# Performance work log

Hardware: AMD Instinct MI355X
Metric: run time of the kernel (lower is better)

## Reference

```python
import jax, jax.numpy as jnp
import numpy as np

LAGRANGE_ORDER = 5  # fixed, as in the torch module


def _lagrange_weights(alpha):
    """Vectorised Lagrange weights of length L+1. alpha: [B,N] -> [B,N,L+1]."""
    L = LAGRANGE_ORDER
    j = jnp.arange(L + 1, dtype=alpha.dtype)
    u = alpha[..., None] - j                          # [B,N,L+1]
    denom = j[:, None] - j[None, :]                   # [L+1,L+1]
    mask = ~jnp.eye(L + 1, dtype=bool)
    num = jnp.where(mask, u[..., None, :], jnp.ones_like(u)[..., None, :])
    den = jnp.where(mask, denom, jnp.ones_like(denom))
    return (num / den).prod(axis=-1)                  # [B,N,L+1]


def setup_inputs() -> dict:
    key = jax.random.key(0)
    k1, k2, k3 = jax.random.split(key, 3)
    B, N = 16, 16384
    # fractional period in samples, in [40, 100) -> max floor(f0)=99, K=99+5+3=107<=108
    f0 = 40.0 + 60.0 * jax.random.uniform(k1, (B, N), dtype=jnp.float32)
    x = jax.random.normal(k2, (B, N), dtype=jnp.float32)
    l_b = jax.random.uniform(k3, (B, N, 2), dtype=jnp.float32)  # (g, p) in [0,1]
    return {"f0": f0, "x": x, "l_b": l_b, "K": 108}


def reference(f0, x, l_b, K):
    B, N = x.shape
    L = LAGRANGE_ORDER
    # design_loop: (g, p) -> loop taps [b0, a1]; gain capped <1 for stability
    g = 0.99 * l_b[..., 0]
    p = l_b[..., 1]
    b0 = g * (1.0 - p)                                # [B,N]
    a1 = g * p
    # tune_f0: subtract low-frequency phase delay of (b0 + a1 z^-1)
    f0c = f0 - a1 / (b0 + a1 + 1e-7)
    # Lagrange centre & weights
    z = jnp.floor(f0c).astype(jnp.int32)
    z_center = z - L // 2                             # [B,N]
    alpha = f0c - z_center.astype(f0.dtype)
    w = _lagrange_weights(alpha)                      # [B,N,L+1]
    # compute_resonator_matrix: loop filter convolved with fractional delay -> block [B,N,L+2]
    block = (b0[..., None] * jnp.pad(w, ((0, 0), (0, 0), (0, 1)))
             + a1[..., None] * jnp.pad(w, ((0, 0), (0, 0), (1, 0))))
    # scatter (-block) into A; LPC lag k+1 lives in column k
    cols = z_center[..., None] - 1 + jnp.arange(L + 2)  # [B,N,L+2]
    cols = jnp.clip(cols, 0, K - 1)
    A = jnp.zeros((B, N, K), x.dtype).at[
        jnp.arange(B)[:, None, None], jnp.arange(N)[None, :, None], cols
    ].add(-block)
    # sample_wise_lpc: y[n] = x[n] - sum_k A[n,k] * y[n-1-k], zero init state
    def step(buf, inp):
        a_n, x_n = inp                                 # [B,K], [B]
        y_n = x_n - jnp.sum(a_n * buf, axis=-1)
        buf = jnp.concatenate([y_n[:, None], buf[:, :-1]], axis=1)
        return buf, y_n
    buf0 = jnp.zeros((B, K), x.dtype)
    _, ys = jax.lax.scan(step, buf0, (A.transpose(1, 0, 2), x.T))  # ys: [N,B]
    return ys.T
```

## Files before the change

### kernel.cpp

```cpp
#include <hip/hip_runtime.h>
#include <math.h>


#define B_    16
#define N_    16384
#define S_    16
#define NSEG  1024
#define NITER 28
#define RUNS  104
#define CHUNK 37

#define TG_FLOATS (B_ * S_ * RUNS * RUNS)
#define ST_FLOATS (B_ * S_ * RUNS)

__device__ __forceinline__ void diffks_coeffs(float f0v, float lbg, float lbp,
                                              int n, float4& lo, float4& hi) {
  float g  = 0.99f * lbg;
  float p  = lbp;
  float b0 = g * (1.0f - p);
  float a1 = g * p;
  float f0c = f0v - a1 / (b0 + a1 + 1e-7f);
  int   zc  = (int)floorf(f0c) - 2;
  float alpha = f0c - (float)zc;
  float u0 = alpha;
  float u1 = alpha - 1.0f;
  float u2 = alpha - 2.0f;
  float u3 = alpha - 3.0f;
  float u4 = alpha - 4.0f;
  float u5 = alpha - 5.0f;
  float w0 = u1 * u2 * u3 * u4 * u5 * (-1.0f / 120.0f);
  float w1 = u0 * u2 * u3 * u4 * u5 * ( 1.0f /  24.0f);
  float w2 = u0 * u1 * u3 * u4 * u5 * (-1.0f /  12.0f);
  float w3 = u0 * u1 * u2 * u4 * u5 * ( 1.0f /  12.0f);
  float w4 = u0 * u1 * u2 * u3 * u5 * (-1.0f /  24.0f);
  float w5 = u0 * u1 * u2 * u3 * u4 * ( 1.0f / 120.0f);
  lo.x = b0 * w0;
  lo.y = fmaf(b0, w1, a1 * w0);
  lo.z = fmaf(b0, w2, a1 * w1);
  lo.w = fmaf(b0, w3, a1 * w2);
  hi.x = fmaf(b0, w4, a1 * w3);
  hi.y = fmaf(b0, w5, a1 * w4);
  hi.z = a1 * w5;
  hi.w = __int_as_float((n - 6 - zc) & 255);
}

__global__ __launch_bounds__(1024) void diffks_phase1(
    const float* __restrict__ f0, const float* __restrict__ lb,
    const float* __restrict__ x, float* __restrict__ Tg) {
  const int bs = blockIdx.x;
  const int b  = bs >> 4, s = bs & 15;
  const int n0 = s << 10;
  const int tid = threadIdx.x;

  __shared__ __align__(16) float hist[256 * RUNS];
  __shared__ float4 sLo[NSEG], sHi[NSEG];
  __shared__ float  sX[NSEG];

  {
    const size_t gi = (size_t)b * N_ + n0 + tid;
    float4 lo, hi;
    diffks_coeffs(f0[gi], lb[2 * gi], lb[2 * gi + 1], tid, lo, hi);
    sLo[tid] = lo; sHi[tid] = hi; sX[tid] = x[gi];
  }
  for (int i = tid; i < 64 * RUNS; i += 1024)
    ((float4*)hist)[i] = float4{0.0f, 0.0f, 0.0f, 0.0f};
  __syncthreads();
  if (tid < 103) hist[(255 - tid) * RUNS + tid] = 1.0f;
  __syncthreads();

  const int w    = tid >> 6;
  const int lane = tid & 63;
  const int cl   = 2 * lane;
  const bool act = (lane < 52);
  const bool px  = (lane == 51);

  for (int t = 0; t < 32; ++t) {
#pragma unroll
    for (int u = 0; u < 2; ++u) {
      const int p = 32 * t + 2 * w + u;
      const float4 lo = sLo[p];
      const float4 hi = sHi[p];
      const float  xv = sX[p];
      if (act) {
        const int base = __float_as_int(hi.w);
        float2 acc;
        acc.x = 0.0f;
        acc.y = px ? xv : 0.0f;
        const float c[7] = {hi.z, hi.y, hi.x, lo.w, lo.z, lo.y, lo.x};
#pragma unroll
        for (int m = 0; m < 7; ++m) {
          const int row = (base + m) & 255;
          const float2 v = *(const float2*)&hist[row * RUNS + cl];
          acc.x = fmaf(c[m], v.x, acc.x);
          acc.y = fmaf(c[m], v.y, acc.y);
        }
        *(float2*)&hist[(p & 255) * RUNS + cl] = acc;
      }
    }
    __syncthreads();
  }

  float* __restrict__ T = Tg + (size_t)bs * RUNS * RUNS;
  for (int idx = tid; idx < RUNS * RUNS; idx += 1024) {
    const int r = idx / RUNS;
    const int j = idx - r * RUNS;
    T[idx] = (j < 103) ? hist[((255 - j) & 255) * RUNS + r] : 0.0f;
  }
}

#define P2_STEP(s_, tv_)                                                      \
  {                                                                           \
    if (q == 0) states[((size_t)b * S_ + (s_)) * RUNS + j] = cur[j];          \
    float acc = 0.0f;                                                         \
    _Pragma("unroll")                                                         \
    for (int k = 0; k < 13; ++k) acc = fmaf(tv_[k], cur[r0 + k], acc);        \
    if ((s_) + 2 < S_) {                                                      \
      const float* __restrict__ Tn = Tb + (size_t)((s_) + 2) * RUNS * RUNS;   \
      _Pragma("unroll")                                                       \
      for (int k = 0; k < 13; ++k) tv_[k] = Tn[(size_t)(r0 + k) * RUNS + j];  \
    }                                                                         \
    part[q][j] = acc;                                                         \
    __syncthreads();                                                          \
    if (q == 0) {                                                             \
      float v = 0.0f;                                                         \
      _Pragma("unroll")                                                       \
      for (int qq = 0; qq < 8; ++qq) v += part[qq][j];                        \
      cur[j] = (j < 103) ? v : 1.0f;                                          \
    }                                                                         \
    __syncthreads();                                                          \
  }

__global__ __launch_bounds__(832) void diffks_phase2(
    const float* __restrict__ Tg, float* __restrict__ states) {
  const int b   = blockIdx.x;
  const int tid = threadIdx.x;
  const int j   = tid % RUNS;
  const int q   = tid / RUNS;
  const int r0  = 13 * q;
  __shared__ float cur[RUNS];
  __shared__ float part[8][105];
  if (tid < 103) cur[tid] = 0.0f;
  if (tid == 103) cur[103] = 1.0f;
  __syncthreads();

  const float* __restrict__ Tb = Tg + (size_t)b * S_ * RUNS * RUNS;
  float tvA[13], tvB[13];
#pragma unroll
  for (int k = 0; k < 13; ++k)
    tvA[k] = Tb[(size_t)(r0 + k) * RUNS + j];
#pragma unroll
  for (int k = 0; k < 13; ++k)
    tvB[k] = Tb[(size_t)RUNS * RUNS + (size_t)(r0 + k) * RUNS + j];

#pragma unroll
  for (int sp = 0; sp < 8; ++sp) {
    P2_STEP(2 * sp,     tvA)
    P2_STEP(2 * sp + 1, tvB)
  }
}

__global__ __launch_bounds__(256) void diffks_phase3(
    const float* __restrict__ f0, const float* __restrict__ lb,
    const float* __restrict__ x, const float* __restrict__ states,
    float* __restrict__ y) {
  const int bs = blockIdx.x;
  const int b  = bs >> 4, s = bs & 15;
  const int n0 = s << 10;
  const int tid = threadIdx.x;

  __shared__ __align__(16) float ring[512];
  __shared__ float4 sC[2 * NSEG];
  __shared__ float  sX[NSEG];
  __shared__ float  sY[NSEG];

#pragma unroll
  for (int k = 0; k < 2; ++k) ring[tid + 256 * k] = 0.0f;
  {
    const size_t gb = (size_t)b * N_ + n0;
    const float*  __restrict__ f0b = f0 + gb;
    const float2* __restrict__ lbb = (const float2*)(lb + 2 * gb);
    const float*  __restrict__ xb  = x + gb;
    float  vf[4]; float2 vl[4]; float vx[4];
#pragma unroll
    for (int k = 0; k < 4; ++k) {
      const int i = tid + 256 * k;
      vf[k] = f0b[i]; vl[k] = lbb[i]; vx[k] = xb[i];
    }
#pragma unroll
    for (int k = 0; k < 4; ++k) {
      const int i = tid + 256 * k;
      float4 lo, hi;
      diffks_coeffs(vf[k], vl[k].x, vl[k].y, n0 + i, lo, hi);
      sC[2 * i] = lo; sC[2 * i + 1] = hi; sX[i] = vx[k];
    }
  }
  __syncthreads();
  const float* __restrict__ st = states + (size_t)bs * RUNS;
  if (tid < 103) {
    const float v = st[tid];
    ring[255 - tid] = v;
    ring[511 - tid] = v;
  }
  __syncthreads();

  if (tid < 64) {
    const int lane = tid;
    const bool act = (lane < CHUNK);
    for (int t = 0; t < NITER; ++t) {
      const int p = t * CHUNK + lane;
      if (act && p < NSEG) {
        const float4 lo = sC[2 * p];
        const float4 hi = sC[2 * p + 1];
        const float  xv = sX[p];
        const int base = __float_as_int(hi.w);
        const float r0 = ring[base + 0];
        const float r1 = ring[base + 1];
        const float r2 = ring[base + 2];
        const float r3 = ring[base + 3];
        const float r4 = ring[base + 4];
        const float r5 = ring[base + 5];
        const float r6 = ring[base + 6];
        const float s0 = fmaf(lo.x, r6, xv);
        const float s1 = fmaf(lo.y, r5, lo.z * r4);
        const float s2 = fmaf(lo.w, r3, hi.x * r2);
        const float s3 = fmaf(hi.y, r1, hi.z * r0);
        const float yv = (s0 + s1) + (s2 + s3);
        const int wsl = p & 255;
        ring[wsl]       = yv;
        ring[wsl + 256] = yv;
        sY[p] = yv;
      }
      __builtin_amdgcn_wave_barrier();
      asm volatile("" ::: "memory");
    }
  }
  __syncthreads();

  float4* __restrict__ yb = (float4*)(y + (size_t)b * N_ + n0);
  yb[tid] = ((const float4*)sY)[tid];
}

__global__ __launch_bounds__(256) void diffks_coeff_fb(
    const float* __restrict__ f0, const float* __restrict__ lb,
    float* __restrict__ cw, int total, int Nmask) {
  int idx = blockIdx.x * blockDim.x + threadIdx.x;
  if (idx >= total) return;
  float4 lo, hi;
  diffks_coeffs(f0[idx], lb[2 * idx], lb[2 * idx + 1], idx & Nmask, lo, hi);
  float4* out4 = (float4*)cw;
  out4[2 * idx]     = lo;
  out4[2 * idx + 1] = hi;
}

__global__ __launch_bounds__(64) void diffks_scan_fb(
    const float* __restrict__ x, const float* __restrict__ cw,
    float* __restrict__ y, int N) {
  const int b    = blockIdx.x;
  const int lane = threadIdx.x;
  __shared__ float ring[512];
#pragma unroll
  for (int i = 0; i < 8; ++i) ring[lane + 64 * i] = 0.0f;
  __builtin_amdgcn_wave_barrier();
  asm volatile("" ::: "memory");
  const float4* __restrict__ c4 = (const float4*)(cw + (size_t)b * N * 8);
  const float*  __restrict__ xb = x + (size_t)b * N;
  float*        __restrict__ yb = y + (size_t)b * N;
  const bool act = (lane < CHUNK);
  const int nIter = (N + CHUNK - 1) / CHUNK;
  for (int t = 0; t < nIter; ++t) {
    const int n = t * CHUNK + lane;
    if (act && n < N) {
      const float4 lo = c4[2 * n];
      const float4 hi = c4[2 * n + 1];
      const float  xv = xb[n];
      const int base = __float_as_int(hi.w);
      const float r0 = ring[base + 0];
      const float r1 = ring[base + 1];
      const float r2 = ring[base + 2];
      const float r3 = ring[base + 3];
      const float r4 = ring[base + 4];
      const float r5 = ring[base + 5];
      const float r6 = ring[base + 6];
      const float s0 = fmaf(lo.x, r6, xv);
      const float s1 = fmaf(lo.y, r5, lo.z * r4);
      const float s2 = fmaf(lo.w, r3, hi.x * r2);
      const float s3 = fmaf(hi.y, r1, hi.z * r0);
      const float yv = (s0 + s1) + (s2 + s3);
      ring[n & 255]         = yv;
      ring[(n & 255) + 256] = yv;
      yb[n] = yv;
    }
    __builtin_amdgcn_wave_barrier();
    asm volatile("" ::: "memory");
  }
}

extern "C" void kernel_launch(void* const* d_in, const int* in_sizes, int n_in,
                              void* d_out, int out_size, void* d_ws, size_t ws_size,
                              hipStream_t stream) {
  const float* f0 = (const float*)d_in[0];
  const float* x  = (const float*)d_in[1];
  const float* lb = (const float*)d_in[2];
  float* out = (float*)d_out;

  const int total = in_sizes[0];
  const size_t need = (size_t)(TG_FLOATS + ST_FLOATS) * 4;

  if (total == B_ * N_ && ws_size >= need) {
    float* Tg = (float*)d_ws;
    float* st = Tg + TG_FLOATS;
    diffks_phase1<<<B_ * S_, 1024, 0, stream>>>(f0, lb, x, Tg);
    diffks_phase2<<<B_, 832, 0, stream>>>(Tg, st);
    diffks_phase3<<<B_ * S_, 256, 0, stream>>>(f0, lb, x, st, out);
  } else {
    const int N = total / B_;
    float* cw = (float*)d_ws;
    diffks_coeff_fb<<<(total + 255) / 256, 256, 0, stream>>>(f0, lb, cw, total, N - 1);
    diffks_scan_fb<<<B_, 64, 0, stream>>>(x, cw, out, N);
  }
}
```

Measured before the change: 104.7 us.

## Fuse three-phase scan into one kernel with global atomic flag handoff

Merges the three kernels (segment transfer matrices, cross-segment state propagation, per-segment final scan) into a single launch of 256 blocks. Blocks signal completion through monotonically increasing global counters compared against snapshots taken at kernel start. The last segment block of each batch runs the state propagation and the other blocks spin-wait for their incoming state. The aim is to remove two kernel launch gaps and reuse the coefficients already held in shared memory. In exchange it relies on all 256 blocks being co-resident to avoid deadlock, and it serializes the phase-2 work onto one block per batch.

Result: slower. 176.1 us (+68.2%).

```diff
diff --git a/kernel.cpp b/kernel.cpp
--- a/kernel.cpp
+++ b/kernel.cpp
@@ -12,6 +12,7 @@
 
 #define TG_FLOATS (B_ * S_ * RUNS * RUNS)
 #define ST_FLOATS (B_ * S_ * RUNS)
+#define NFLAGS    512
 
 __device__ __forceinline__ void diffks_coeffs(float f0v, float lbg, float lbp,
                                               int n, float4& lo, float4& hi) {
@@ -44,84 +45,26 @@
   hi.w = __int_as_float((n - 6 - zc) & 255);
 }
 
-__global__ __launch_bounds__(1024) void diffks_phase1(
-    const float* __restrict__ f0, const float* __restrict__ lb,
-    const float* __restrict__ x, float* __restrict__ Tg) {
-  const int bs = blockIdx.x;
-  const int b  = bs >> 4, s = bs & 15;
-  const int n0 = s << 10;
-  const int tid = threadIdx.x;
-
-  __shared__ __align__(16) float hist[256 * RUNS];
-  __shared__ float4 sLo[NSEG], sHi[NSEG];
-  __shared__ float  sX[NSEG];
-
-  {
-    const size_t gi = (size_t)b * N_ + n0 + tid;
-    float4 lo, hi;
-    diffks_coeffs(f0[gi], lb[2 * gi], lb[2 * gi + 1], tid, lo, hi);
-    sLo[tid] = lo; sHi[tid] = hi; sX[tid] = x[gi];
-  }
-  for (int i = tid; i < 64 * RUNS; i += 1024)
-    ((float4*)hist)[i] = float4{0.0f, 0.0f, 0.0f, 0.0f};
-  __syncthreads();
-  if (tid < 103) hist[(255 - tid) * RUNS + tid] = 1.0f;
-  __syncthreads();
-
-  const int w    = tid >> 6;
-  const int lane = tid & 63;
-  const int cl   = 2 * lane;
-  const bool act = (lane < 52);
-  const bool px  = (lane == 51);
-
-  for (int t = 0; t < 32; ++t) {
-#pragma unroll
-    for (int u = 0; u < 2; ++u) {
-      const int p = 32 * t + 2 * w + u;
-      const float4 lo = sLo[p];
-      const float4 hi = sHi[p];
-      const float  xv = sX[p];
-      if (act) {
-        const int base = __float_as_int(hi.w);
-        float2 acc;
-        acc.x = 0.0f;
-        acc.y = px ? xv : 0.0f;
-        const float c[7] = {hi.z, hi.y, hi.x, lo.w, lo.z, lo.y, lo.x};
-#pragma unroll
-        for (int m = 0; m < 7; ++m) {
-          const int row = (base + m) & 255;
-          const float2 v = *(const float2*)&hist[row * RUNS + cl];
-          acc.x = fmaf(c[m], v.x, acc.x);
-          acc.y = fmaf(c[m], v.y, acc.y);
-        }
-        *(float2*)&hist[(p & 255) * RUNS + cl] = acc;
-      }
-    }
-    __syncthreads();
-  }
-
-  float* __restrict__ T = Tg + (size_t)bs * RUNS * RUNS;
-  for (int idx = tid; idx < RUNS * RUNS; idx += 1024) {
-    const int r = idx / RUNS;
-    const int j = idx - r * RUNS;
-    T[idx] = (j < 103) ? hist[((255 - j) & 255) * RUNS + r] : 0.0f;
-  }
-}
-
-#define P2_STEP(s_, tv_)                                                      \
+#define P2F_STEP(s_, tv_)                                                     \
   {                                                                           \
-    if (q == 0) states[((size_t)b * S_ + (s_)) * RUNS + j] = cur[j];          \
-    float acc = 0.0f;                                                         \
-    _Pragma("unroll")                                                         \
-    for (int k = 0; k < 13; ++k) acc = fmaf(tv_[k], cur[r0 + k], acc);        \
-    if ((s_) + 2 < S_) {                                                      \
-      const float* __restrict__ Tn = Tb + (size_t)((s_) + 2) * RUNS * RUNS;   \
+    if (p2a) {                                                                \
+      if (q == 0) states[((size_t)b * S_ + (s_)) * RUNS + j] = cur[j];        \
+      float acc = 0.0f;                                                       \
       _Pragma("unroll")                                                       \
-      for (int k = 0; k < 13; ++k) tv_[k] = Tn[(size_t)(r0 + k) * RUNS + j];  \
+      for (int k = 0; k < 13; ++k) acc = fmaf(tv_[k], cur[r0 + k], acc);      \
+      if ((s_) + 2 < S_) {                                                    \
+        const float* __restrict__ Tn = Tb + (size_t)((s_) + 2) * RUNS * RUNS; \
+        _Pragma("unroll")                                                     \
+        for (int k = 0; k < 13; ++k) tv_[k] = Tn[(size_t)(r0 + k) * RUNS + j];\
+      }                                                                       \
+      part[q][j] = acc;                                                       \
     }                                                                         \
-    part[q][j] = acc;                                                         \
     __syncthreads();                                                          \
-    if (q == 0) {                                                             \
+    if (tid == 0) {                                                           \
+      __threadfence();                                                        \
+      atomicAdd(&flagS[(b << 4) + (s_)], 1u);                                 \
+    }                                                                         \
+    if (p2a && q == 0) {                                                      \
       float v = 0.0f;                                                         \
       _Pragma("unroll")                                                       \
       for (int qq = 0; qq < 8; ++qq) v += part[qq][j];                        \
@@ -130,87 +73,161 @@
     __syncthreads();                                                          \
   }
 
-__global__ __launch_bounds__(832) void diffks_phase2(
-    const float* __restrict__ Tg, float* __restrict__ states) {
-  const int b   = blockIdx.x;
-  const int tid = threadIdx.x;
-  const int j   = tid % RUNS;
-  const int q   = tid / RUNS;
-  const int r0  = 13 * q;
-  __shared__ float cur[RUNS];
-  __shared__ float part[8][105];
-  if (tid < 103) cur[tid] = 0.0f;
-  if (tid == 103) cur[103] = 1.0f;
-  __syncthreads();
-
-  const float* __restrict__ Tb = Tg + (size_t)b * S_ * RUNS * RUNS;
-  float tvA[13], tvB[13];
-#pragma unroll
-  for (int k = 0; k < 13; ++k)
-    tvA[k] = Tb[(size_t)(r0 + k) * RUNS + j];
-#pragma unroll
-  for (int k = 0; k < 13; ++k)
-    tvB[k] = Tb[(size_t)RUNS * RUNS + (size_t)(r0 + k) * RUNS + j];
-
-#pragma unroll
-  for (int sp = 0; sp < 8; ++sp) {
-    P2_STEP(2 * sp,     tvA)
-    P2_STEP(2 * sp + 1, tvB)
-  }
-}
-
-__global__ __launch_bounds__(256) void diffks_phase3(
+__global__ __launch_bounds__(1024) void diffks_fused(
     const float* __restrict__ f0, const float* __restrict__ lb,
-    const float* __restrict__ x, const float* __restrict__ states,
-    float* __restrict__ y) {
+    const float* __restrict__ x, float* __restrict__ Tg,
+    float* __restrict__ states, unsigned* __restrict__ flagT,
+    unsigned* __restrict__ flagS, float* __restrict__ y) {
   const int bs = blockIdx.x;
   const int b  = bs >> 4, s = bs & 15;
   const int n0 = s << 10;
   const int tid = threadIdx.x;
 
-  __shared__ __align__(16) float ring[512];
-  __shared__ float4 sC[2 * NSEG];
+  __shared__ __align__(16) float hist[256 * RUNS];
+  __shared__ __align__(16) float4 sLo[NSEG], sHi[NSEG];
   __shared__ float  sX[NSEG];
-  __shared__ float  sY[NSEG];
-
-#pragma unroll
-  for (int k = 0; k < 2; ++k) ring[tid + 256 * k] = 0.0f;
+  __shared__ unsigned snapT[16];
+
+  unsigned snapS = 0u;
+  if (tid == 0)
+    snapS = __hip_atomic_load(&flagS[bs], __ATOMIC_RELAXED,
+                              __HIP_MEMORY_SCOPE_AGENT);
+  if (tid < 16)
+    snapT[tid] = __hip_atomic_load(&flagT[(b << 4) + tid], __ATOMIC_RELAXED,
+                                   __HIP_MEMORY_SCOPE_AGENT);
+
   {
-    const size_t gb = (size_t)b * N_ + n0;
-    const float*  __restrict__ f0b = f0 + gb;
-    const float2* __restrict__ lbb = (const float2*)(lb + 2 * gb);
-    const float*  __restrict__ xb  = x + gb;
-    float  vf[4]; float2 vl[4]; float vx[4];
-#pragma unroll
-    for (int k = 0; k < 4; ++k) {
-      const int i = tid + 256 * k;
-      vf[k] = f0b[i]; vl[k] = lbb[i]; vx[k] = xb[i];
-    }
-#pragma unroll
-    for (int k = 0; k < 4; ++k) {
-      const int i = tid + 256 * k;
-      float4 lo, hi;
-      diffks_coeffs(vf[k], vl[k].x, vl[k].y, n0 + i, lo, hi);
-      sC[2 * i] = lo; sC[2 * i + 1] = hi; sX[i] = vx[k];
-    }
-  }
-  __syncthreads();
-  const float* __restrict__ st = states + (size_t)bs * RUNS;
-  if (tid < 103) {
-    const float v = st[tid];
-    ring[255 - tid] = v;
-    ring[511 - tid] = v;
+    const size_t gi = (size_t)b * N_ + n0 + tid;
+    float4 lo, hi;
+    diffks_coeffs(f0[gi], lb[2 * gi], lb[2 * gi + 1], tid, lo, hi);
+    sLo[tid] = lo; sHi[tid] = hi; sX[tid] = x[gi];
+  }
+  for (int i = tid; i < 64 * RUNS; i += 1024)
+    ((float4*)hist)[i] = float4{0.0f, 0.0f, 0.0f, 0.0f};
+  __syncthreads();
+  if (tid < 103) hist[(255 - tid) * RUNS + tid] = 1.0f;
+  __syncthreads();
+
+  {
+    const int w    = tid >> 6;
+    const int lane = tid & 63;
+    const int cl   = 2 * lane;
+    const bool act = (lane < 52);
+    const bool px  = (lane == 51);
+
+    for (int t = 0; t < 32; ++t) {
+#pragma unroll
+      for (int u = 0; u < 2; ++u) {
+        const int p = 32 * t + 2 * w + u;
+        const float4 lo = sLo[p];
+        const float4 hi = sHi[p];
+        const float  xv = sX[p];
+        if (act) {
+          const int base = __float_as_int(hi.w);
+          float2 acc;
+          acc.x = 0.0f;
+          acc.y = px ? xv : 0.0f;
+          const float c[7] = {hi.z, hi.y, hi.x, lo.w, lo.z, lo.y, lo.x};
+#pragma unroll
+          for (int m = 0; m < 7; ++m) {
+            const int row = (base + m) & 255;
+            const float2 v = *(const float2*)&hist[row * RUNS + cl];
+            acc.x = fmaf(c[m], v.x, acc.x);
+            acc.y = fmaf(c[m], v.y, acc.y);
+          }
+          *(float2*)&hist[(p & 255) * RUNS + cl] = acc;
+        }
+      }
+      __syncthreads();
+    }
+  }
+
+  {
+    float* __restrict__ T = Tg + (size_t)bs * RUNS * RUNS;
+    for (int idx = tid; idx < RUNS * RUNS; idx += 1024) {
+      const int r = idx / RUNS;
+      const int j = idx - r * RUNS;
+      T[idx] = (j < 103) ? hist[((255 - j) & 255) * RUNS + r] : 0.0f;
+    }
+  }
+  __syncthreads();
+  if (tid == 0) {
+    __threadfence();
+    atomicAdd(&flagT[bs], 1u);
+  }
+
+  if (tid < 512) hist[tid] = 0.0f;
+
+  if (s == 15) {
+    if (tid == 0) {
+      for (int i = 0; i < 16; ++i) {
+        while (__hip_atomic_load(&flagT[(b << 4) + i], __ATOMIC_RELAXED,
+                                 __HIP_MEMORY_SCOPE_AGENT) == snapT[i])
+          __builtin_amdgcn_s_sleep(1);
+      }
+      __threadfence();
+    }
+    __syncthreads();
+
+    const int j   = tid % RUNS;
+    const int q   = tid / RUNS;
+    const int r0  = 13 * q;
+    const bool p2a = (tid < 832);
+    float* __restrict__ cur = hist + 1536;
+    float (*__restrict__ part)[105] = (float (*)[105])(hist + 1664);
+
+    if (tid < 103) cur[tid] = 0.0f;
+    if (tid == 103) cur[103] = 1.0f;
+    __syncthreads();
+
+    const float* __restrict__ Tb = Tg + (size_t)b * S_ * RUNS * RUNS;
+    float tvA[13], tvB[13];
+    if (p2a) {
+#pragma unroll
+      for (int k = 0; k < 13; ++k)
+        tvA[k] = Tb[(size_t)(r0 + k) * RUNS + j];
+#pragma unroll
+      for (int k = 0; k < 13; ++k)
+        tvB[k] = Tb[(size_t)RUNS * RUNS + (size_t)(r0 + k) * RUNS + j];
+    }
+
+#pragma unroll
+    for (int sp = 0; sp < 8; ++sp) {
+      P2F_STEP(2 * sp,     tvA)
+      P2F_STEP(2 * sp + 1, tvB)
+    }
+  }
+
+  if (s != 15 && s != 0) {
+    if (tid == 0) {
+      while (__hip_atomic_load(&flagS[bs], __ATOMIC_RELAXED,
+                               __HIP_MEMORY_SCOPE_AGENT) == snapS)
+        __builtin_amdgcn_s_sleep(1);
+      __threadfence();
+    }
+  }
+  __syncthreads();
+
+  if (s != 0) {
+    const float* __restrict__ st = states + (size_t)bs * RUNS;
+    if (tid < 103) {
+      const float v = st[tid];
+      hist[255 - tid] = v;
+      hist[511 - tid] = v;
+    }
   }
   __syncthreads();
 
   if (tid < 64) {
     const int lane = tid;
     const bool act = (lane < CHUNK);
+    float* __restrict__ ring = hist;
+    float* __restrict__ sY   = hist + 512;
     for (int t = 0; t < NITER; ++t) {
       const int p = t * CHUNK + lane;
       if (act && p < NSEG) {
-        const float4 lo = sC[2 * p];
-        const float4 hi = sC[2 * p + 1];
+        const float4 lo = sLo[p];
+        const float4 hi = sHi[p];
         const float  xv = sX[p];
         const int base = __float_as_int(hi.w);
         const float r0 = ring[base + 0];
@@ -236,8 +253,10 @@
   }
   __syncthreads();
 
-  float4* __restrict__ yb = (float4*)(y + (size_t)b * N_ + n0);
-  yb[tid] = ((const float4*)sY)[tid];
+  if (tid < 256) {
+    float4* __restrict__ yb = (float4*)(y + (size_t)b * N_ + n0);
+    yb[tid] = ((const float4*)(hist + 512))[tid];
+  }
 }
 
 __global__ __launch_bounds__(256) void diffks_coeff_fb(
@@ -304,14 +323,14 @@
   float* out = (float*)d_out;
 
   const int total = in_sizes[0];
-  const size_t need = (size_t)(TG_FLOATS + ST_FLOATS) * 4;
+  const size_t need = (size_t)(TG_FLOATS + ST_FLOATS) * 4 + NFLAGS * 4;
 
   if (total == B_ * N_ && ws_size >= need) {
     float* Tg = (float*)d_ws;
     float* st = Tg + TG_FLOATS;
-    diffks_phase1<<<B_ * S_, 1024, 0, stream>>>(f0, lb, x, Tg);
-    diffks_phase2<<<B_, 832, 0, stream>>>(Tg, st);
-    diffks_phase3<<<B_ * S_, 256, 0, stream>>>(f0, lb, x, st, out);
+    unsigned* flagT = (unsigned*)(st + ST_FLOATS);
+    unsigned* flagS = flagT + 256;
+    diffks_fused<<<B_ * S_, 1024, 0, stream>>>(f0, lb, x, Tg, st, flagT, flagS, out);
   } else {
     const int N = total / B_;
     float* cw = (float*)d_ws;
```

## Cache filter coefficients in phase1 for phase3 and pad history ring to avoid wraps

Applied to the files above, without the earlier changes.

Phase1 now writes the per-sample Lagrange/loop coefficients it computes to a workspace buffer, and phase3 loads them instead of recomputing from f0 and l_b. The phase1 history buffer gains 7 mirror rows so the 7-tap reads need no per-tap modulo masking, at the cost of a duplicate store when the write slot is below 7. It also loads l_b as float2. The trade is extra global traffic (32 bytes per sample written and read) against removing the coefficient math and index masking.

Result: slower. 110.5 us (+5.6%).

```diff
diff --git a/kernel.cpp b/kernel.cpp
--- a/kernel.cpp
+++ b/kernel.cpp
@@ -9,9 +9,11 @@
 #define NITER 28
 #define RUNS  104
 #define CHUNK 37
+#define HROWS 263
 
 #define TG_FLOATS (B_ * S_ * RUNS * RUNS)
 #define ST_FLOATS (B_ * S_ * RUNS)
+#define CG_FLOATS (B_ * S_ * NSEG * 8)
 
 __device__ __forceinline__ void diffks_coeffs(float f0v, float lbg, float lbp,
                                               int n, float4& lo, float4& hi) {
@@ -46,58 +48,69 @@
 
 __global__ __launch_bounds__(1024) void diffks_phase1(
     const float* __restrict__ f0, const float* __restrict__ lb,
-    const float* __restrict__ x, float* __restrict__ Tg) {
+    const float* __restrict__ x, float* __restrict__ Tg,
+    float* __restrict__ Cg) {
   const int bs = blockIdx.x;
   const int b  = bs >> 4, s = bs & 15;
   const int n0 = s << 10;
   const int tid = threadIdx.x;
 
-  __shared__ __align__(16) float hist[256 * RUNS];
+  __shared__ __align__(16) float hist[HROWS * RUNS];
   __shared__ float4 sLo[NSEG], sHi[NSEG];
   __shared__ float  sX[NSEG];
 
   {
     const size_t gi = (size_t)b * N_ + n0 + tid;
+    const float2 lv = ((const float2*)lb)[gi];
     float4 lo, hi;
-    diffks_coeffs(f0[gi], lb[2 * gi], lb[2 * gi + 1], tid, lo, hi);
+    diffks_coeffs(f0[gi], lv.x, lv.y, tid, lo, hi);
     sLo[tid] = lo; sHi[tid] = hi; sX[tid] = x[gi];
-  }
-  for (int i = tid; i < 64 * RUNS; i += 1024)
+    float4* __restrict__ C = (float4*)Cg + (size_t)bs * 2 * NSEG;
+    C[2 * tid]     = lo;
+    C[2 * tid + 1] = hi;
+  }
+  for (int i = tid; i < (HROWS * RUNS) / 4; i += 1024)
     ((float4*)hist)[i] = float4{0.0f, 0.0f, 0.0f, 0.0f};
   __syncthreads();
   if (tid < 103) hist[(255 - tid) * RUNS + tid] = 1.0f;
   __syncthreads();
 
-  const int w    = tid >> 6;
-  const int lane = tid & 63;
-  const int cl   = 2 * lane;
-  const bool act = (lane < 52);
-  const bool px  = (lane == 51);
-
-  for (int t = 0; t < 32; ++t) {
-#pragma unroll
-    for (int u = 0; u < 2; ++u) {
-      const int p = 32 * t + 2 * w + u;
-      const float4 lo = sLo[p];
-      const float4 hi = sHi[p];
-      const float  xv = sX[p];
-      if (act) {
-        const int base = __float_as_int(hi.w);
-        float2 acc;
-        acc.x = 0.0f;
-        acc.y = px ? xv : 0.0f;
-        const float c[7] = {hi.z, hi.y, hi.x, lo.w, lo.z, lo.y, lo.x};
-#pragma unroll
-        for (int m = 0; m < 7; ++m) {
-          const int row = (base + m) & 255;
-          const float2 v = *(const float2*)&hist[row * RUNS + cl];
-          acc.x = fmaf(c[m], v.x, acc.x);
-          acc.y = fmaf(c[m], v.y, acc.y);
+  {
+    const int w    = tid >> 6;
+    const int lane = tid & 63;
+    const int cl   = 2 * lane;
+    const bool act = (lane < 52);
+    const bool px  = (lane == 51);
+    float* __restrict__ hcol = hist + cl;
+
+    for (int t = 0; t < 32; ++t) {
+#pragma unroll
+      for (int u = 0; u < 2; ++u) {
+        const int p = 32 * t + 2 * w + u;
+        const float4 lo = sLo[p];
+        const float4 hi = sHi[p];
+        const float  xv = sX[p];
+        if (act) {
+          const int base = __float_as_int(hi.w);
+          const float* __restrict__ hr = hcol + base * RUNS;
+          float2 acc;
+          acc.x = 0.0f;
+          acc.y = px ? xv : 0.0f;
+          const float c[7] = {hi.z, hi.y, hi.x, lo.w, lo.z, lo.y, lo.x};
+#pragma unroll
+          for (int m = 0; m < 7; ++m) {
+            const float2 v = *(const float2*)(hr + m * RUNS);
+            acc.x = fmaf(c[m], v.x, acc.x);
+            acc.y = fmaf(c[m], v.y, acc.y);
+          }
+          const int wsl = p & 255;
+          *(float2*)(hcol + wsl * RUNS) = acc;
+          if (wsl < 7)
+            *(float2*)(hcol + (wsl + 256) * RUNS) = acc;
         }
-        *(float2*)&hist[(p & 255) * RUNS + cl] = acc;
       }
-    }
-    __syncthreads();
+      __syncthreads();
+    }
   }
 
   float* __restrict__ T = Tg + (size_t)bs * RUNS * RUNS;
@@ -160,9 +173,8 @@
 }
 
 __global__ __launch_bounds__(256) void diffks_phase3(
-    const float* __restrict__ f0, const float* __restrict__ lb,
-    const float* __restrict__ x, const float* __restrict__ states,
-    float* __restrict__ y) {
+    const float* __restrict__ Cg, const float* __restrict__ x,
+    const float* __restrict__ states, float* __restrict__ y) {
   const int bs = blockIdx.x;
   const int b  = bs >> 4, s = bs & 15;
   const int n0 = s << 10;
@@ -177,21 +189,18 @@
   for (int k = 0; k < 2; ++k) ring[tid + 256 * k] = 0.0f;
   {
     const size_t gb = (size_t)b * N_ + n0;
-    const float*  __restrict__ f0b = f0 + gb;
-    const float2* __restrict__ lbb = (const float2*)(lb + 2 * gb);
-    const float*  __restrict__ xb  = x + gb;
-    float  vf[4]; float2 vl[4]; float vx[4];
+    const float*  __restrict__ xb = x + gb;
+    const float4* __restrict__ cb = (const float4*)Cg + (size_t)bs * 2 * NSEG;
+    float4 v0[4], v1[4]; float vx[4];
 #pragma unroll
     for (int k = 0; k < 4; ++k) {
       const int i = tid + 256 * k;
-      vf[k] = f0b[i]; vl[k] = lbb[i]; vx[k] = xb[i];
+      v0[k] = cb[2 * i]; v1[k] = cb[2 * i + 1]; vx[k] = xb[i];
     }
 #pragma unroll
     for (int k = 0; k < 4; ++k) {
       const int i = tid + 256 * k;
-      float4 lo, hi;
-      diffks_coeffs(vf[k], vl[k].x, vl[k].y, n0 + i, lo, hi);
-      sC[2 * i] = lo; sC[2 * i + 1] = hi; sX[i] = vx[k];
+      sC[2 * i] = v0[k]; sC[2 * i + 1] = v1[k]; sX[i] = vx[k];
     }
   }
   __syncthreads();
@@ -304,14 +313,15 @@
   float* out = (float*)d_out;
 
   const int total = in_sizes[0];
-  const size_t need = (size_t)(TG_FLOATS + ST_FLOATS) * 4;
+  const size_t need = (size_t)(TG_FLOATS + ST_FLOATS + CG_FLOATS) * 4;
 
   if (total == B_ * N_ && ws_size >= need) {
     float* Tg = (float*)d_ws;
     float* st = Tg + TG_FLOATS;
-    diffks_phase1<<<B_ * S_, 1024, 0, stream>>>(f0, lb, x, Tg);
+    float* Cg = st + ST_FLOATS;
+    diffks_phase1<<<B_ * S_, 1024, 0, stream>>>(f0, lb, x, Tg, Cg);
     diffks_phase2<<<B_, 832, 0, stream>>>(Tg, st);
-    diffks_phase3<<<B_ * S_, 256, 0, stream>>>(f0, lb, x, st, out);
+    diffks_phase3<<<B_ * S_, 256, 0, stream>>>(Cg, x, st, out);
   } else {
     const int N = total / B_;
     float* cw = (float*)d_ws;
```

## Split phase1 transfer-matrix build across two half-column blocks with register-held coefficients

Applied to the files above, without the earlier changes.

Phase1 now launches twice as many 512-thread blocks, each computing half of the 104 basis columns, which halves the shared-memory history per block and allows more blocks per CU. Per-sample coefficients are kept in registers and broadcast with readlane instead of being staged in shared memory. Each lane now updates four columns with float4 loads across four samples per wave, and a small row-wrap mirror replaces the modulo row indexing. This is meant to raise occupancy and cut LDS traffic in the serial recurrence. In exchange the coefficient math is duplicated across both halves, and the readlane broadcasts and select logic add scalar and ALU work.

New measurement: 129.0 us. 1.23x slower.

```diff
diff --git a/kernel.cpp b/kernel.cpp
--- a/kernel.cpp
+++ b/kernel.cpp
@@ -8,10 +8,14 @@
 #define NSEG  1024
 #define NITER 28
 #define RUNS  104
+#define RUNS_H 52
 #define CHUNK 37
+#define HROWS 263
 
 #define TG_FLOATS (B_ * S_ * RUNS * RUNS)
 #define ST_FLOATS (B_ * S_ * RUNS)
+
+#define RL(v, l) __int_as_float(__builtin_amdgcn_readlane(__float_as_int(v), (l)))
 
 __device__ __forceinline__ void diffks_coeffs(float f0v, float lbg, float lbp,
                                               int n, float4& lo, float4& hi) {
@@ -44,67 +48,128 @@
   hi.w = __int_as_float((n - 6 - zc) & 255);
 }
 
-__global__ __launch_bounds__(1024) void diffks_phase1(
+__global__ __launch_bounds__(512, 4) void diffks_phase1(
     const float* __restrict__ f0, const float* __restrict__ lb,
     const float* __restrict__ x, float* __restrict__ Tg) {
-  const int bs = blockIdx.x;
+  const int bs2 = blockIdx.x;
+  const int bs = bs2 >> 1, h = bs2 & 1;
   const int b  = bs >> 4, s = bs & 15;
   const int n0 = s << 10;
   const int tid = threadIdx.x;
-
-  __shared__ __align__(16) float hist[256 * RUNS];
-  __shared__ float4 sLo[NSEG], sHi[NSEG];
-  __shared__ float  sX[NSEG];
-
-  {
-    const size_t gi = (size_t)b * N_ + n0 + tid;
-    float4 lo, hi;
-    diffks_coeffs(f0[gi], lb[2 * gi], lb[2 * gi + 1], tid, lo, hi);
-    sLo[tid] = lo; sHi[tid] = hi; sX[tid] = x[gi];
-  }
-  for (int i = tid; i < 64 * RUNS; i += 1024)
-    ((float4*)hist)[i] = float4{0.0f, 0.0f, 0.0f, 0.0f};
-  __syncthreads();
-  if (tid < 103) hist[(255 - tid) * RUNS + tid] = 1.0f;
-  __syncthreads();
-
   const int w    = tid >> 6;
   const int lane = tid & 63;
-  const int cl   = 2 * lane;
-  const bool act = (lane < 52);
-  const bool px  = (lane == 51);
-
-  for (int t = 0; t < 32; ++t) {
-#pragma unroll
-    for (int u = 0; u < 2; ++u) {
-      const int p = 32 * t + 2 * w + u;
-      const float4 lo = sLo[p];
-      const float4 hi = sHi[p];
-      const float  xv = sX[p];
+
+  __shared__ __align__(16) float hist[HROWS * RUNS_H];
+
+  float4 cLoA, cHiA, cLoB, cHiB; float cXA, cXB;
+  {
+    const int pA = 32 * (lane & 31) + 4 * w + (lane >> 5);
+    const int pB = pA + 2;
+    const size_t gA = (size_t)b * N_ + n0 + pA;
+    const size_t gB = (size_t)b * N_ + n0 + pB;
+    const float2 lvA = ((const float2*)lb)[gA];
+    const float2 lvB = ((const float2*)lb)[gB];
+    diffks_coeffs(f0[gA], lvA.x, lvA.y, pA, cLoA, cHiA);
+    diffks_coeffs(f0[gB], lvB.x, lvB.y, pB, cLoB, cHiB);
+    cXA = x[gA]; cXB = x[gB];
+  }
+
+  {
+    float4* __restrict__ hz = (float4*)(hist + 152 * RUNS_H);
+    for (int i = tid; i < 104 * RUNS_H / 4; i += 512)
+      hz[i] = float4{0.0f, 0.0f, 0.0f, 0.0f};
+  }
+  __syncthreads();
+  if (tid < RUNS_H && (h == 0 || tid < 51))
+    hist[(255 - (RUNS_H * h + tid)) * RUNS_H + tid] = 1.0f;
+  __syncthreads();
+
+  {
+    const int  g   = lane / 13;
+    const int  q   = lane - 13 * g;
+    const bool act = (lane < 52);
+    const bool s1  = (g & 1) != 0;
+    const bool s2  = (g & 2) != 0;
+    const bool px  = act && (q == 12) && (h == 1);
+    float* __restrict__ hq = hist + 4 * q;
+
+#define SEL4(a0, a1, a2, a3) (s2 ? (s1 ? (a3) : (a2)) : (s1 ? (a1) : (a0)))
+
+    for (int t = 0; t < 32; ++t) {
+      const int lA = t, lB = t + 32;
+      const float b6_0 = RL(cHiA.z, lA), b6_1 = RL(cHiA.z, lB),
+                  b6_2 = RL(cHiB.z, lA), b6_3 = RL(cHiB.z, lB);
+      const float b5_0 = RL(cHiA.y, lA), b5_1 = RL(cHiA.y, lB),
+                  b5_2 = RL(cHiB.y, lA), b5_3 = RL(cHiB.y, lB);
+      const float b4_0 = RL(cHiA.x, lA), b4_1 = RL(cHiA.x, lB),
+                  b4_2 = RL(cHiB.x, lA), b4_3 = RL(cHiB.x, lB);
+      const float b3_0 = RL(cLoA.w, lA), b3_1 = RL(cLoA.w, lB),
+                  b3_2 = RL(cLoB.w, lA), b3_3 = RL(cLoB.w, lB);
+      const float b2_0 = RL(cLoA.z, lA), b2_1 = RL(cLoA.z, lB),
+                  b2_2 = RL(cLoB.z, lA), b2_3 = RL(cLoB.z, lB);
+      const float b1_0 = RL(cLoA.y, lA), b1_1 = RL(cLoA.y, lB),
+                  b1_2 = RL(cLoB.y, lA), b1_3 = RL(cLoB.y, lB);
+      const float b0_0 = RL(cLoA.x, lA), b0_1 = RL(cLoA.x, lB),
+                  b0_2 = RL(cLoB.x, lA), b0_3 = RL(cLoB.x, lB);
+      const float bw_0 = RL(cHiA.w, lA), bw_1 = RL(cHiA.w, lB),
+                  bw_2 = RL(cHiB.w, lA), bw_3 = RL(cHiB.w, lB);
+      const float x_0  = RL(cXA,   lA), x_1  = RL(cXA,   lB),
+                  x_2  = RL(cXB,   lA), x_3  = RL(cXB,   lB);
+
       if (act) {
-        const int base = __float_as_int(hi.w);
-        float2 acc;
-        acc.x = 0.0f;
-        acc.y = px ? xv : 0.0f;
-        const float c[7] = {hi.z, hi.y, hi.x, lo.w, lo.z, lo.y, lo.x};
-#pragma unroll
-        for (int m = 0; m < 7; ++m) {
-          const int row = (base + m) & 255;
-          const float2 v = *(const float2*)&hist[row * RUNS + cl];
-          acc.x = fmaf(c[m], v.x, acc.x);
-          acc.y = fmaf(c[m], v.y, acc.y);
+        const float c0 = SEL4(b6_0, b6_1, b6_2, b6_3);
+        const float c1 = SEL4(b5_0, b5_1, b5_2, b5_3);
+        const float c2 = SEL4(b4_0, b4_1, b4_2, b4_3);
+        const float c3 = SEL4(b3_0, b3_1, b3_2, b3_3);
+        const float c4 = SEL4(b2_0, b2_1, b2_2, b2_3);
+        const float c5 = SEL4(b1_0, b1_1, b1_2, b1_3);
+        const float c6 = SEL4(b0_0, b0_1, b0_2, b0_3);
+        const int   base = __float_as_int(SEL4(bw_0, bw_1, bw_2, bw_3));
+        const float xv   = SEL4(x_0, x_1, x_2, x_3);
+
+        const float4* __restrict__ hr = (const float4*)(hq + base * RUNS_H);
+        float4 a;
+        a.x = 0.0f; a.y = 0.0f; a.z = 0.0f;
+        a.w = px ? xv : 0.0f;
+        {
+          const float4 v0 = hr[0 * 13];
+          const float4 v1 = hr[1 * 13];
+          const float4 v2 = hr[2 * 13];
+          const float4 v3 = hr[3 * 13];
+          const float4 v4 = hr[4 * 13];
+          const float4 v5 = hr[5 * 13];
+          const float4 v6 = hr[6 * 13];
+          a.x = fmaf(c0, v0.x, a.x); a.y = fmaf(c0, v0.y, a.y);
+          a.z = fmaf(c0, v0.z, a.z); a.w = fmaf(c0, v0.w, a.w);
+          a.x = fmaf(c1, v1.x, a.x); a.y = fmaf(c1, v1.y, a.y);
+          a.z = fmaf(c1, v1.z, a.z); a.w = fmaf(c1, v1.w, a.w);
+          a.x = fmaf(c2, v2.x, a.x); a.y = fmaf(c2, v2.y, a.y);
+          a.z = fmaf(c2, v2.z, a.z); a.w = fmaf(c2, v2.w, a.w);
+          a.x = fmaf(c3, v3.x, a.x); a.y = fmaf(c3, v3.y, a.y);
+          a.z = fmaf(c3, v3.z, a.z); a.w = fmaf(c3, v3.w, a.w);
+          a.x = fmaf(c4, v4.x, a.x); a.y = fmaf(c4, v4.y, a.y);
+          a.z = fmaf(c4, v4.z, a.z); a.w = fmaf(c4, v4.w, a.w);
+          a.x = fmaf(c5, v5.x, a.x); a.y = fmaf(c5, v5.y, a.y);
+          a.z = fmaf(c5, v5.z, a.z); a.w = fmaf(c5, v5.w, a.w);
+          a.x = fmaf(c6, v6.x, a.x); a.y = fmaf(c6, v6.y, a.y);
+          a.z = fmaf(c6, v6.z, a.z); a.w = fmaf(c6, v6.w, a.w);
         }
-        *(float2*)&hist[(p & 255) * RUNS + cl] = acc;
+        const int p   = 32 * t + 4 * w + g;
+        const int wsl = p & 255;
+        *(float4*)(hq + wsl * RUNS_H) = a;
+        if (((t & 7) == 0) && (w < 2) && (wsl < 7))
+          *(float4*)(hq + (wsl + 256) * RUNS_H) = a;
       }
-    }
-    __syncthreads();
-  }
-
-  float* __restrict__ T = Tg + (size_t)bs * RUNS * RUNS;
-  for (int idx = tid; idx < RUNS * RUNS; idx += 1024) {
-    const int r = idx / RUNS;
-    const int j = idx - r * RUNS;
-    T[idx] = (j < 103) ? hist[((255 - j) & 255) * RUNS + r] : 0.0f;
+      __syncthreads();
+    }
+#undef SEL4
+  }
+
+  float* __restrict__ T = Tg + ((size_t)bs * RUNS + RUNS_H * h) * RUNS;
+  for (int idx = tid; idx < RUNS_H * RUNS; idx += 512) {
+    const int rl = idx / RUNS;
+    const int j  = idx - rl * RUNS;
+    T[idx] = (j < 103) ? hist[(255 - j) * RUNS_H + rl] : 0.0f;
   }
 }
 
@@ -309,7 +374,7 @@
   if (total == B_ * N_ && ws_size >= need) {
     float* Tg = (float*)d_ws;
     float* st = Tg + TG_FLOATS;
-    diffks_phase1<<<B_ * S_, 1024, 0, stream>>>(f0, lb, x, Tg);
+    diffks_phase1<<<2 * B_ * S_, 512, 0, stream>>>(f0, lb, x, Tg);
     diffks_phase2<<<B_, 832, 0, stream>>>(Tg, st);
     diffks_phase3<<<B_ * S_, 256, 0, stream>>>(f0, lb, x, st, out);
   } else {
```
